# Kernel tuning notes

Hardware: AMD Instinct MI355X
Metric: run time of the kernel (lower is better)

## Reference

```python
import jax, jax.numpy as jnp
import numpy as np

OUT_FEATURES = 11008
IN_FEATURES = 4096
GROUP_SIZE = 128
NUM_GROUPS = OUT_FEATURES * IN_FEATURES // GROUP_SIZE  # 352256

NF4_VALUES = jnp.array([
    -1.0, -0.6961928009986877, -0.5250730514526367, -0.39491748809814453,
    -0.28444138169288635, -0.18477343022823334, -0.09105003625154495, 0.0,
    0.07958029955625534, 0.16093020141124725, 0.24611230194568634,
    0.33791524171829224, 0.44070982933044434, 0.5626170039176941,
    0.7229568362236023, 1.0], dtype=jnp.float32)


def setup_inputs() -> dict:
    key = jax.random.key(0)
    k1, k2, k3, k4 = jax.random.split(key, 4)
    x = jax.random.normal(k1, (4, 2048, IN_FEATURES), dtype=jnp.float32)
    weight_quant = jax.random.randint(k2, (OUT_FEATURES * IN_FEATURES,), 0, 16, dtype=jnp.int32)
    weight_scale = jax.random.uniform(k3, (NUM_GROUPS,), dtype=jnp.float32) * 0.05 + 1e-3
    bias = jax.random.normal(k4, (OUT_FEATURES,), dtype=jnp.float32)
    return {"x": x, "weight_quant": weight_quant, "weight_scale": weight_scale, "bias": bias}


def reference(x, weight_quant, weight_scale, bias):
    # NF4 dequantization: table lookup, then per-group (of 128 consecutive flat
    # elements) scale multiply, then reshape to [out_features, in_features].
    idx = jnp.clip(weight_quant, 0, 15)
    w = NF4_VALUES.astype(x.dtype)[idx]                      # flat [OUT*IN]
    w = (w.reshape(NUM_GROUPS, GROUP_SIZE)
         * weight_scale.astype(x.dtype)[:, None])
    w = w.reshape(OUT_FEATURES, IN_FEATURES)
    # F.linear: x @ W^T + b
    out = jnp.einsum('bsi,oi->bso', x, w) + bias.astype(x.dtype)
    return out
```

## Files before the change

### kernel.cpp

```cpp
#include <hip/hip_runtime.h>
#include <hip/hip_bf16.h>
#include <stdint.h>
#include <stddef.h>

#define OUT_F  11008
#define IN_F   4096
#define M_ROWS 8192

typedef __bf16 bf16;
typedef __attribute__((ext_vector_type(8))) __bf16 bf16x8;
typedef __attribute__((ext_vector_type(4))) float floatx4;

__device__ const float NF4_TAB[16] = {
    -1.0f, -0.6961928009986877f, -0.5250730514526367f, -0.39491748809814453f,
    -0.28444138169288635f, -0.18477343022823334f, -0.09105003625154495f, 0.0f,
    0.07958029955625534f, 0.16093020141124725f, 0.24611230194568634f,
    0.33791524171829224f, 0.44070982933044434f, 0.5626170039176941f,
    0.7229568362236023f, 1.0f};

__global__ __launch_bounds__(256) void cvt_x_kernel(const float* __restrict__ x,
                                                    bf16* __restrict__ xb) {
    size_t t = (size_t)blockIdx.x * 256 + threadIdx.x;
    const float4* xv = (const float4*)x;
    float4 a = xv[2 * t];
    float4 b = xv[2 * t + 1];
    bf16x8 o;
    o[0] = (bf16)a.x; o[1] = (bf16)a.y; o[2] = (bf16)a.z; o[3] = (bf16)a.w;
    o[4] = (bf16)b.x; o[5] = (bf16)b.y; o[6] = (bf16)b.z; o[7] = (bf16)b.w;
    *(bf16x8*)(xb + 8 * t) = o;
}

__global__ __launch_bounds__(256) void dequant_kernel(const int* __restrict__ q,
                                                      const float* __restrict__ sc,
                                                      bf16* __restrict__ wb) {
    __shared__ float tab[16];
    if (threadIdx.x < 16) tab[threadIdx.x] = NF4_TAB[threadIdx.x];
    __syncthreads();
    size_t t = (size_t)blockIdx.x * 256 + threadIdx.x;
    const int4* qv = (const int4*)q;
    int4 a = qv[2 * t];
    int4 b = qv[2 * t + 1];
    float s = sc[t >> 4];
    bf16x8 o;
    o[0] = (bf16)(tab[a.x & 15] * s); o[1] = (bf16)(tab[a.y & 15] * s);
    o[2] = (bf16)(tab[a.z & 15] * s); o[3] = (bf16)(tab[a.w & 15] * s);
    o[4] = (bf16)(tab[b.x & 15] * s); o[5] = (bf16)(tab[b.y & 15] * s);
    o[6] = (bf16)(tab[b.z & 15] * s); o[7] = (bf16)(tab[b.w & 15] * s);
    *(bf16x8*)(wb + 8 * t) = o;
}

#define BM 128
#define BN 128
#define BK 32

static __device__ __forceinline__ void gload_lds16(const void* g, void* l) {
    __builtin_amdgcn_global_load_lds((const __attribute__((address_space(1))) void*)g,
                                     (__attribute__((address_space(3))) void*)l,
                                     16, 0, 0);
}

__global__ __launch_bounds__(256) void gemm_bias_kernel(const bf16* __restrict__ A,
                                                        const bf16* __restrict__ B,
                                                        const float* __restrict__ bias,
                                                        float* __restrict__ C) {
    __shared__ bf16 sA[BM * BK];
    __shared__ bf16 sB[BN * BK];

    const int tid  = threadIdx.x;
    const int wv   = tid >> 6;
    const int lane = tid & 63;
    const int quad = lane >> 4;
    const int l16  = lane & 15;

    const int bm = blockIdx.y * BM;
    const int bn = blockIdx.x * BN;

    const int srow = lane >> 2;
    const int scol = (lane & 3) * 8;

    const int wm = (wv >> 1) * 64;
    const int wn = (wv & 1) * 64;

    floatx4 acc[4][4] = {};

    const bf16* Abase = A + (size_t)bm * IN_F;
    const bf16* Bbase = B + (size_t)bn * IN_F;

    for (int k0 = 0; k0 < IN_F; k0 += BK) {
#pragma unroll
        for (int i = 0; i < 2; ++i) {
            int row = i * 64 + wv * 16 + srow;
            gload_lds16(Abase + (size_t)row * IN_F + k0 + scol,
                        &sA[(i * 64 + wv * 16) * BK]);
        }
#pragma unroll
        for (int i = 0; i < 2; ++i) {
            int row = i * 64 + wv * 16 + srow;
            gload_lds16(Bbase + (size_t)row * IN_F + k0 + scol,
                        &sB[(i * 64 + wv * 16) * BK]);
        }
        __syncthreads();

        bf16x8 af[4], bfr[4];
#pragma unroll
        for (int mt = 0; mt < 4; ++mt)
            af[mt] = *(const bf16x8*)&sA[(wm + mt * 16 + l16) * BK + quad * 8];
#pragma unroll
        for (int nt = 0; nt < 4; ++nt)
            bfr[nt] = *(const bf16x8*)&sB[(wn + nt * 16 + l16) * BK + quad * 8];
#pragma unroll
        for (int mt = 0; mt < 4; ++mt)
#pragma unroll
            for (int nt = 0; nt < 4; ++nt)
                acc[mt][nt] = __builtin_amdgcn_mfma_f32_16x16x32_bf16(
                    af[mt], bfr[nt], acc[mt][nt], 0, 0, 0);
        __syncthreads();
    }

#pragma unroll
    for (int nt = 0; nt < 4; ++nt) {
        int col = bn + wn + nt * 16 + l16;
        float bv = bias[col];
#pragma unroll
        for (int mt = 0; mt < 4; ++mt) {
            int row0 = bm + wm + mt * 16 + quad * 4;
#pragma unroll
            for (int r = 0; r < 4; ++r)
                C[(size_t)(row0 + r) * OUT_F + col] = acc[mt][nt][r] + bv;
        }
    }
}

#define FBM 64
#define FBN 64
#define FBK 64
__global__ __launch_bounds__(256) void fallback_gemm(const float* __restrict__ x,
                                                     const int* __restrict__ q,
                                                     const float* __restrict__ sc,
                                                     const float* __restrict__ bias,
                                                     float* __restrict__ out) {
    __shared__ float sA[FBM][FBK + 1];
    __shared__ float sB[FBN][FBK + 1];
    const int tx = threadIdx.x & 15, ty = threadIdx.x >> 4;
    const int bm = blockIdx.y * FBM, bn = blockIdx.x * FBN;
    float acc[4][4] = {};
    for (int k0 = 0; k0 < IN_F; k0 += FBK) {
        for (int i = threadIdx.x; i < FBM * (FBK / 4); i += 256) {
            int r = i / (FBK / 4), c4 = (i % (FBK / 4)) * 4;
            float4 v = *(const float4*)&x[(size_t)(bm + r) * IN_F + k0 + c4];
            sA[r][c4] = v.x; sA[r][c4 + 1] = v.y; sA[r][c4 + 2] = v.z; sA[r][c4 + 3] = v.w;
            size_t fi = (size_t)(bn + r) * IN_F + k0 + c4;
            int4 qv = *(const int4*)&q[fi];
            float s = sc[fi >> 7];
            sB[r][c4]     = NF4_TAB[qv.x & 15] * s;
            sB[r][c4 + 1] = NF4_TAB[qv.y & 15] * s;
            sB[r][c4 + 2] = NF4_TAB[qv.z & 15] * s;
            sB[r][c4 + 3] = NF4_TAB[qv.w & 15] * s;
        }
        __syncthreads();
        for (int k = 0; k < FBK; ++k) {
            float av[4], bvv[4];
#pragma unroll
            for (int i = 0; i < 4; ++i) av[i] = sA[ty * 4 + i][k];
#pragma unroll
            for (int j = 0; j < 4; ++j) bvv[j] = sB[tx * 4 + j][k];
#pragma unroll
            for (int i = 0; i < 4; ++i)
#pragma unroll
                for (int j = 0; j < 4; ++j) acc[i][j] += av[i] * bvv[j];
        }
        __syncthreads();
    }
#pragma unroll
    for (int i = 0; i < 4; ++i)
#pragma unroll
        for (int j = 0; j < 4; ++j)
            out[(size_t)(bm + ty * 4 + i) * OUT_F + bn + tx * 4 + j] =
                acc[i][j] + bias[bn + tx * 4 + j];
}

extern "C" void kernel_launch(void* const* d_in, const int* in_sizes, int n_in,
                              void* d_out, int out_size, void* d_ws, size_t ws_size,
                              hipStream_t stream) {
    const float* x    = (const float*)d_in[0];
    const int*   q    = (const int*)d_in[1];
    const float* sc   = (const float*)d_in[2];
    const float* bias = (const float*)d_in[3];
    float* out = (float*)d_out;

    const size_t xb_bytes = (size_t)M_ROWS * IN_F * sizeof(bf16);
    const size_t wb_bytes = (size_t)OUT_F * IN_F * sizeof(bf16);

    if (ws_size >= xb_bytes + wb_bytes) {
        bf16* xb = (bf16*)d_ws;
        bf16* wb = (bf16*)((char*)d_ws + xb_bytes);
        cvt_x_kernel<<<(M_ROWS * IN_F) / (8 * 256), 256, 0, stream>>>(x, xb);
        dequant_kernel<<<(OUT_F * IN_F) / (8 * 256), 256, 0, stream>>>(q, sc, wb);
        gemm_bias_kernel<<<dim3(OUT_F / BN, M_ROWS / BM), 256, 0, stream>>>(xb, wb, bias, out);
    } else {
        fallback_gemm<<<dim3(OUT_F / FBN, M_ROWS / FBM), 256, 0, stream>>>(x, q, sc, bias, out);
    }
}
```

Baseline: 1.486 ms.

## Enlarge GEMM tiles to 256x256 with 4-stage LDS pipeline and swizzles

Rewrites the bf16 GEMM to use 256x256 block tiles with 512 threads and a four-deep LDS ring buffer. Global-to-LDS loads are issued three stages ahead using vmcnt-based waits and a single barrier per k-step. The change also adds an XOR swizzle on LDS columns to avoid bank conflicts, a block-index remap for L2 locality, and s_setprio around the MFMA bursts. The goal is to hide memory latency and raise arithmetic intensity, at the cost of heavier register use (8x4 accumulators per wave) and tighter LDS usage.

New measurement: 1.539 ms. +3.6%, slower.

```diff
diff --git a/kernel.cpp b/kernel.cpp
--- a/kernel.cpp
+++ b/kernel.cpp
@@ -49,9 +49,11 @@
     *(bf16x8*)(wb + 8 * t) = o;
 }
 
-#define BM 128
-#define BN 128
+#define BM 256
+#define BN 256
 #define BK 32
+#define NT (IN_F / BK)
+#define GRID ((M_ROWS / BM) * (OUT_F / BN))
 
 static __device__ __forceinline__ void gload_lds16(const void* g, void* l) {
     __builtin_amdgcn_global_load_lds((const __attribute__((address_space(1))) void*)g,
@@ -59,71 +61,108 @@
                                      16, 0, 0);
 }
 
-__global__ __launch_bounds__(256) void gemm_bias_kernel(const bf16* __restrict__ A,
-                                                        const bf16* __restrict__ B,
-                                                        const float* __restrict__ bias,
-                                                        float* __restrict__ C) {
-    __shared__ bf16 sA[BM * BK];
-    __shared__ bf16 sB[BN * BK];
+__global__ __launch_bounds__(512, 2) void gemm_bias_kernel(const bf16* __restrict__ A,
+                                                           const bf16* __restrict__ B,
+                                                           const float* __restrict__ bias,
+                                                           float* __restrict__ C) {
+    __shared__ bf16 sA[4][BM * BK];
+    __shared__ bf16 sB[4][BN * BK];
 
     const int tid  = threadIdx.x;
-    const int wv   = tid >> 6;
+    const int w    = tid >> 6;
     const int lane = tid & 63;
+    const int wm   = w >> 2;
+    const int wn   = w & 3;
+    const int l16  = lane & 15;
     const int quad = lane >> 4;
-    const int l16  = lane & 15;
-
-    const int bm = blockIdx.y * BM;
-    const int bn = blockIdx.x * BN;
-
-    const int srow = lane >> 2;
-    const int scol = (lane & 3) * 8;
-
-    const int wm = (wv >> 1) * 64;
-    const int wn = (wv & 1) * 64;
-
-    floatx4 acc[4][4] = {};
-
-    const bf16* Abase = A + (size_t)bm * IN_F;
-    const bf16* Bbase = B + (size_t)bn * IN_F;
-
-    for (int k0 = 0; k0 < IN_F; k0 += BK) {
-#pragma unroll
-        for (int i = 0; i < 2; ++i) {
-            int row = i * 64 + wv * 16 + srow;
-            gload_lds16(Abase + (size_t)row * IN_F + k0 + scol,
-                        &sA[(i * 64 + wv * 16) * BK]);
-        }
-#pragma unroll
-        for (int i = 0; i < 2; ++i) {
-            int row = i * 64 + wv * 16 + srow;
-            gload_lds16(Bbase + (size_t)row * IN_F + k0 + scol,
-                        &sB[(i * 64 + wv * 16) * BK]);
-        }
-        __syncthreads();
-
-        bf16x8 af[4], bfr[4];
-#pragma unroll
-        for (int mt = 0; mt < 4; ++mt)
-            af[mt] = *(const bf16x8*)&sA[(wm + mt * 16 + l16) * BK + quad * 8];
+
+    const int bid = blockIdx.x;
+    const int swz = (bid & 7) * (GRID / 8) + (bid >> 3);
+    const int tm  = swz / (OUT_F / BN);
+    const int tn  = swz % (OUT_F / BN);
+    const int bm  = tm * BM;
+    const int bn  = tn * BN;
+
+    const int lr = lane >> 2;
+    const int ls = (lane & 3) ^ (lr & 3);
+    const bf16* aG = A + (size_t)(bm + w * 32 + lr) * IN_F + ls * 8;
+    const bf16* bG = B + (size_t)(bn + w * 32 + lr) * IN_F + ls * 8;
+
+    const int soff = (quad ^ (l16 & 3)) * 8;
+    const int aOff = (wm * 128 + l16) * BK + soff;
+    const int bOff = (wn * 64 + l16) * BK + soff;
+
+    floatx4 acc[8][4] = {};
+
+    auto stage = [&](int tt) {
+        bf16* la = &sA[tt & 3][w * 1024];
+        bf16* lb = &sB[tt & 3][w * 1024];
+        const bf16* ga = aG + (size_t)tt * BK;
+        const bf16* gb = bG + (size_t)tt * BK;
+        gload_lds16(ga, la);
+        gload_lds16(ga + (size_t)16 * IN_F, la + 512);
+        gload_lds16(gb, lb);
+        gload_lds16(gb + (size_t)16 * IN_F, lb + 512);
+    };
+
+    auto compute = [&](int t) {
+        const bf16* bufA = sA[t & 3];
+        const bf16* bufB = sB[t & 3];
+        bf16x8 bfrg[4], afrg[4];
 #pragma unroll
         for (int nt = 0; nt < 4; ++nt)
-            bfr[nt] = *(const bf16x8*)&sB[(wn + nt * 16 + l16) * BK + quad * 8];
+            bfrg[nt] = *(const bf16x8*)(bufB + bOff + nt * 512);
+#pragma unroll
+        for (int mt = 0; mt < 4; ++mt)
+            afrg[mt] = *(const bf16x8*)(bufA + aOff + mt * 512);
+        asm volatile("s_waitcnt lgkmcnt(0)" ::: "memory");
+        __builtin_amdgcn_s_setprio(1);
 #pragma unroll
         for (int mt = 0; mt < 4; ++mt)
 #pragma unroll
             for (int nt = 0; nt < 4; ++nt)
                 acc[mt][nt] = __builtin_amdgcn_mfma_f32_16x16x32_bf16(
-                    af[mt], bfr[nt], acc[mt][nt], 0, 0, 0);
-        __syncthreads();
-    }
+                    afrg[mt], bfrg[nt], acc[mt][nt], 0, 0, 0);
+        __builtin_amdgcn_s_setprio(0);
+#pragma unroll
+        for (int mt = 0; mt < 4; ++mt)
+            afrg[mt] = *(const bf16x8*)(bufA + aOff + (mt + 4) * 512);
+        asm volatile("s_waitcnt lgkmcnt(0)" ::: "memory");
+        __builtin_amdgcn_s_setprio(1);
+#pragma unroll
+        for (int mt = 0; mt < 4; ++mt)
+#pragma unroll
+            for (int nt = 0; nt < 4; ++nt)
+                acc[mt + 4][nt] = __builtin_amdgcn_mfma_f32_16x16x32_bf16(
+                    afrg[mt], bfrg[nt], acc[mt + 4][nt], 0, 0, 0);
+        __builtin_amdgcn_s_setprio(0);
+    };
+
+    stage(0); stage(1); stage(2);
+
+    for (int t = 0; t < NT - 3; ++t) {
+        asm volatile("s_waitcnt vmcnt(8)" ::: "memory");
+        __builtin_amdgcn_s_barrier();
+        stage(t + 3);
+        compute(t);
+    }
+    asm volatile("s_waitcnt vmcnt(8)" ::: "memory");
+    __builtin_amdgcn_s_barrier();
+    compute(NT - 3);
+    asm volatile("s_waitcnt vmcnt(4)" ::: "memory");
+    __builtin_amdgcn_s_barrier();
+    compute(NT - 2);
+    asm volatile("s_waitcnt vmcnt(0)" ::: "memory");
+    __builtin_amdgcn_s_barrier();
+    compute(NT - 1);
 
 #pragma unroll
     for (int nt = 0; nt < 4; ++nt) {
-        int col = bn + wn + nt * 16 + l16;
+        int col = bn + wn * 64 + nt * 16 + l16;
         float bv = bias[col];
 #pragma unroll
-        for (int mt = 0; mt < 4; ++mt) {
-            int row0 = bm + wm + mt * 16 + quad * 4;
+        for (int mt = 0; mt < 8; ++mt) {
+            int row0 = bm + wm * 128 + mt * 16 + quad * 4;
 #pragma unroll
             for (int r = 0; r < 4; ++r)
                 C[(size_t)(row0 + r) * OUT_F + col] = acc[mt][nt][r] + bv;
@@ -196,7 +235,7 @@
         bf16* wb = (bf16*)((char*)d_ws + xb_bytes);
         cvt_x_kernel<<<(M_ROWS * IN_F) / (8 * 256), 256, 0, stream>>>(x, xb);
         dequant_kernel<<<(OUT_F * IN_F) / (8 * 256), 256, 0, stream>>>(q, sc, wb);
-        gemm_bias_kernel<<<dim3(OUT_F / BN, M_ROWS / BM), 256, 0, stream>>>(xb, wb, bias, out);
+        gemm_bias_kernel<<<GRID, 512, 0, stream>>>(xb, wb, bias, out);
     } else {
         fallback_gemm<<<dim3(OUT_F / FBN, M_ROWS / FBM), 256, 0, stream>>>(x, q, sc, bias, out);
     }
```
